# Performance work log

Measured on AMD Instinct MI355X. Metric: run time of the kernel, lower is better.

The kernel has to match this reference:

```python
import jax, jax.numpy as jnp
import numpy as np

B, C, H, W = 4, 192, 128, 128
HEADS = 4

def _conv1x1(x, w):
    # x: [B,Cin,H,W], w: [Cout,Cin,1,1]
    return jnp.einsum('bchw,oc->bohw', x, w[:, :, 0, 0])

def _dwconv3x3(x, w):
    # x: [B,C3,H,W], w: [C3,1,3,3], groups=C3
    return jax.lax.conv_general_dilated(
        x, w, window_strides=(1, 1), padding=((1, 1), (1, 1)),
        dimension_numbers=('NCHW', 'OIHW', 'NCHW'),
        feature_group_count=x.shape[1])

def setup_inputs() -> dict:
    key = jax.random.key(0)
    k1, k2, k3, k4 = jax.random.split(key, 4)
    return {
        'x': jax.random.normal(k1, (B, C, H, W), jnp.float32),
        'w_qkv': jax.random.normal(k2, (3 * C, C, 1, 1), jnp.float32) * 0.05,
        'w_dw': jax.random.normal(k3, (3 * C, 1, 3, 3), jnp.float32) * 0.1,
        'w_proj': jax.random.normal(k4, (C, C, 1, 1), jnp.float32) * 0.05,
        'temperature': jnp.ones((HEADS, 1, 1), jnp.float32),
    }

def reference(x, w_qkv, w_dw, w_proj, temperature):
    b, c, h, w = x.shape
    ch = c // HEADS  # channels per head
    qkv = _dwconv3x3(_conv1x1(x, w_qkv), w_dw)  # [B,3C,H,W]
    q, k, v = jnp.split(qkv, 3, axis=1)
    def heads(t):  # [B,C,H,W] -> [B,heads,ch,HW]
        return t.reshape(b, HEADS, ch, h * w)
    q, k, v = heads(q), heads(k), heads(v)
    # L2 normalize over spatial (token) axis
    q = q / jnp.maximum(jnp.linalg.norm(q, axis=-1, keepdims=True), 1e-12)
    k = k / jnp.maximum(jnp.linalg.norm(k, axis=-1, keepdims=True), 1e-12)
    attn = jnp.einsum('bhcn,bhdn->bhcd', q, k) * temperature[None]  # [B,heads,ch,ch]
    attn = jax.nn.softmax(attn, axis=-1)
    out = jnp.einsum('bhcd,bhdn->bhcn', attn, v)  # [B,heads,ch,HW]
    out = out.reshape(b, c, h, w)
    return _conv1x1(out, w_proj)
```

## Files before the change

kernel.cpp:

```cpp
#include <hip/hip_runtime.h>
#include <hip/hip_bf16.h>
#include <math.h>


#define B_ 4
#define C_ 192
#define H_ 128
#define W_ 128
#define HW_ 16384
#define HEADS_ 4
#define CH_ 48
#define CHUNKS_ 64

typedef __attribute__((ext_vector_type(8))) __bf16 bf16x8;
typedef __attribute__((ext_vector_type(8))) unsigned short u16x8;
typedef __attribute__((ext_vector_type(4))) float f32x4;

__device__ __forceinline__ unsigned short rne_bf16(float f) {
    unsigned int u = __float_as_uint(f);
    u += 0x7FFFu + ((u >> 16) & 1u);
    return (unsigned short)(u >> 16);
}
__device__ __forceinline__ float bf16_f32(unsigned short h) {
    return __uint_as_float(((unsigned int)h) << 16);
}

__global__ void k0_bf16(const float* __restrict__ wq,
                        unsigned short* __restrict__ wB, int n) {
    int idx = blockIdx.x * 256 + threadIdx.x;
    if (idx < n) wB[idx] = rne_bf16(wq[idx]);
}

__global__ __launch_bounds__(256, 3) void kg_f32(
    const unsigned short* __restrict__ A, int aStrideB,
    const float* __restrict__ X, unsigned short* __restrict__ Y) {
    __shared__ unsigned short AL[2][64 * 40];
    __shared__ unsigned short BL[2][256 * 40];
    int t = threadIdx.x;
    int wave = t >> 6, lane = t & 63;
    int lm = lane & 15, kg = lane >> 4;
    int p0 = blockIdx.x * 256;
    int m0 = blockIdx.y * 64;
    int b = blockIdx.z;
    const unsigned short* Ab = A + (size_t)b * aStrideB + (size_t)m0 * C_;
    const float* Xb = X + (size_t)b * C_ * HW_ + p0 + t;
    int ar = t >> 2, ac = (t & 3) * 8;
    size_t arow = (size_t)ar * C_ + ac;

    f32x4 acc[4][4];
#pragma unroll
    for (int mi = 0; mi < 4; ++mi)
#pragma unroll
        for (int ni = 0; ni < 4; ++ni) acc[mi][ni] = (f32x4)(0.f);

    float xv[32];
    u16x8 av;
#pragma unroll
    for (int i = 0; i < 32; ++i) xv[i] = Xb[(size_t)i * HW_];
    av = *(const u16x8*)&Ab[arow];
    *(u16x8*)&AL[0][ar * 40 + ac] = av;
#pragma unroll
    for (int c8 = 0; c8 < 4; ++c8) {
        u16x8 hh;
#pragma unroll
        for (int j = 0; j < 8; ++j) hh[j] = rne_bf16(xv[c8 * 8 + j]);
        *(u16x8*)&BL[0][t * 40 + c8 * 8] = hh;
    }
    __syncthreads();

    for (int s = 0; s < 6; ++s) {
        int cur = s & 1;
        if (s < 5) {
            int kn = (s + 1) * 32;
            const float* xp = Xb + (size_t)kn * HW_;
#pragma unroll
            for (int i = 0; i < 32; ++i) xv[i] = xp[(size_t)i * HW_];
            av = *(const u16x8*)&Ab[arow + kn];
        }
        bf16x8 fah[4], fbh[4];
#pragma unroll
        for (int mi = 0; mi < 4; ++mi) {
            int ro = (lm + mi * 16) * 40 + kg * 8;
            fah[mi] = __builtin_bit_cast(bf16x8, *(const u16x8*)&AL[cur][ro]);
        }
#pragma unroll
        for (int ni = 0; ni < 4; ++ni) {
            int ro = (wave * 64 + ni * 16 + lm) * 40 + kg * 8;
            fbh[ni] = __builtin_bit_cast(bf16x8, *(const u16x8*)&BL[cur][ro]);
        }
#pragma unroll
        for (int mi = 0; mi < 4; ++mi)
#pragma unroll
            for (int ni = 0; ni < 4; ++ni)
                acc[mi][ni] = __builtin_amdgcn_mfma_f32_16x16x32_bf16(
                    fah[mi], fbh[ni], acc[mi][ni], 0, 0, 0);
        if (s < 5) {
            int nxt = cur ^ 1;
            *(u16x8*)&AL[nxt][ar * 40 + ac] = av;
#pragma unroll
            for (int c8 = 0; c8 < 4; ++c8) {
                u16x8 hh;
#pragma unroll
                for (int j = 0; j < 8; ++j) hh[j] = rne_bf16(xv[c8 * 8 + j]);
                *(u16x8*)&BL[nxt][t * 40 + c8 * 8] = hh;
            }
        }
        __syncthreads();
    }
#pragma unroll
    for (int mi = 0; mi < 4; ++mi)
#pragma unroll
        for (int ni = 0; ni < 4; ++ni) {
            int oc = m0 + mi * 16 + kg * 4;
            int px = p0 + wave * 64 + ni * 16 + lm;
            unsigned short* yp = Y + ((size_t)b * C_ + oc) * HW_ + px;
#pragma unroll
            for (int r = 0; r < 4; ++r)
                yp[(size_t)r * HW_] = rne_bf16(acc[mi][ni][r]);
        }
}

__global__ __launch_bounds__(256, 3) void kg_b16(
    const unsigned short* __restrict__ A, int aStrideB,
    const unsigned short* __restrict__ X, float* __restrict__ Y) {
    __shared__ unsigned short AL[2][64 * 40];
    __shared__ unsigned short BL[2][256 * 40];
    int t = threadIdx.x;
    int wave = t >> 6, lane = t & 63;
    int lm = lane & 15, kg = lane >> 4;
    int p0 = blockIdx.x * 256;
    int m0 = blockIdx.y * 64;
    int b = blockIdx.z;
    const unsigned short* Ab = A + (size_t)b * aStrideB + (size_t)m0 * C_;
    const unsigned short* Xb = X + (size_t)b * C_ * HW_ + p0 + t;
    int ar = t >> 2, ac = (t & 3) * 8;
    size_t arow = (size_t)ar * C_ + ac;

    f32x4 acc[4][4];
#pragma unroll
    for (int mi = 0; mi < 4; ++mi)
#pragma unroll
        for (int ni = 0; ni < 4; ++ni) acc[mi][ni] = (f32x4)(0.f);

    unsigned short xv[32];
    u16x8 av;
#pragma unroll
    for (int i = 0; i < 32; ++i) xv[i] = Xb[(size_t)i * HW_];
    av = *(const u16x8*)&Ab[arow];
    *(u16x8*)&AL[0][ar * 40 + ac] = av;
#pragma unroll
    for (int c8 = 0; c8 < 4; ++c8) {
        u16x8 hh;
#pragma unroll
        for (int j = 0; j < 8; ++j) hh[j] = xv[c8 * 8 + j];
        *(u16x8*)&BL[0][t * 40 + c8 * 8] = hh;
    }
    __syncthreads();

    for (int s = 0; s < 6; ++s) {
        int cur = s & 1;
        if (s < 5) {
            int kn = (s + 1) * 32;
            const unsigned short* xp = Xb + (size_t)kn * HW_;
#pragma unroll
            for (int i = 0; i < 32; ++i) xv[i] = xp[(size_t)i * HW_];
            av = *(const u16x8*)&Ab[arow + kn];
        }
        bf16x8 fah[4], fbh[4];
#pragma unroll
        for (int mi = 0; mi < 4; ++mi) {
            int ro = (lm + mi * 16) * 40 + kg * 8;
            fah[mi] = __builtin_bit_cast(bf16x8, *(const u16x8*)&AL[cur][ro]);
        }
#pragma unroll
        for (int ni = 0; ni < 4; ++ni) {
            int ro = (wave * 64 + ni * 16 + lm) * 40 + kg * 8;
            fbh[ni] = __builtin_bit_cast(bf16x8, *(const u16x8*)&BL[cur][ro]);
        }
#pragma unroll
        for (int mi = 0; mi < 4; ++mi)
#pragma unroll
            for (int ni = 0; ni < 4; ++ni)
                acc[mi][ni] = __builtin_amdgcn_mfma_f32_16x16x32_bf16(
                    fah[mi], fbh[ni], acc[mi][ni], 0, 0, 0);
        if (s < 5) {
            int nxt = cur ^ 1;
            *(u16x8*)&AL[nxt][ar * 40 + ac] = av;
#pragma unroll
            for (int c8 = 0; c8 < 4; ++c8) {
                u16x8 hh;
#pragma unroll
                for (int j = 0; j < 8; ++j) hh[j] = xv[c8 * 8 + j];
                *(u16x8*)&BL[nxt][t * 40 + c8 * 8] = hh;
            }
        }
        __syncthreads();
    }
#pragma unroll
    for (int mi = 0; mi < 4; ++mi)
#pragma unroll
        for (int ni = 0; ni < 4; ++ni) {
            int oc = m0 + mi * 16 + kg * 4;
            int px = p0 + wave * 64 + ni * 16 + lm;
            float* yp = Y + ((size_t)b * C_ + oc) * HW_ + px;
#pragma unroll
            for (int r = 0; r < 4; ++r) yp[(size_t)r * HW_] = acc[mi][ni][r];
        }
}

__global__ __launch_bounds__(256, 6) void k2_dwconv(
    const unsigned short* __restrict__ y1, const float* __restrict__ wdw,
    unsigned short* __restrict__ dst, float* __restrict__ ssP, int g) {
    __shared__ float wss[4];
    int t = threadIdx.x;
    int c = blockIdx.y, b = blockIdx.z;
    int cg = (t & 31) * 4;
    int r0i = blockIdx.x * 32 + (t >> 5) * 4;
    const unsigned short* yp = y1 + ((size_t)b * C_ + c) * HW_;
    const float* wd = wdw + (size_t)(g * C_ + c) * 9;
    float w0 = wd[0], w1 = wd[1], w2 = wd[2];
    float w3 = wd[3], w4 = wd[4], w5 = wd[5];
    float w6 = wd[6], w7 = wd[7], w8 = wd[8];
    bool lv = cg > 0, rv = cg < W_ - 4;

    float4 mid[6];
    float lf[6], rt[6];
#pragma unroll
    for (int i = 0; i < 6; ++i) {
        int rr = r0i - 1 + i;
        if (rr >= 0 && rr < H_) {
            const unsigned short* rowp = yp + (size_t)rr * W_;
            ushort4 mv = *(const ushort4*)&rowp[cg];
            mid[i] = make_float4(bf16_f32(mv.x), bf16_f32(mv.y),
                                 bf16_f32(mv.z), bf16_f32(mv.w));
            lf[i] = lv ? bf16_f32(rowp[cg - 1]) : 0.f;
            rt[i] = rv ? bf16_f32(rowp[cg + 4]) : 0.f;
        } else {
            mid[i] = make_float4(0.f, 0.f, 0.f, 0.f);
            lf[i] = 0.f;
            rt[i] = 0.f;
        }
    }
    float ss = 0.f;
#pragma unroll
    for (int i = 0; i < 4; ++i) {
        float o0 = 0.f, o1 = 0.f, o2 = 0.f, o3 = 0.f;
#pragma unroll
        for (int k = 0; k < 3; ++k) {
            float4 m = mid[i + k];
            float L = lf[i + k], R = rt[i + k];
            float wa = (k == 0) ? w0 : (k == 1) ? w3 : w6;
            float wb = (k == 0) ? w1 : (k == 1) ? w4 : w7;
            float wc = (k == 0) ? w2 : (k == 1) ? w5 : w8;
            o0 = fmaf(wa, L,   fmaf(wb, m.x, fmaf(wc, m.y, o0)));
            o1 = fmaf(wa, m.x, fmaf(wb, m.y, fmaf(wc, m.z, o1)));
            o2 = fmaf(wa, m.y, fmaf(wb, m.z, fmaf(wc, m.w, o2)));
            o3 = fmaf(wa, m.z, fmaf(wb, m.w, fmaf(wc, R,   o3)));
        }
        unsigned short h0 = rne_bf16(o0), h1 = rne_bf16(o1);
        unsigned short h2 = rne_bf16(o2), h3 = rne_bf16(o3);
        float f0 = bf16_f32(h0), f1 = bf16_f32(h1);
        float f2 = bf16_f32(h2), f3 = bf16_f32(h3);
        ss += f0 * f0 + f1 * f1 + f2 * f2 + f3 * f3;
        size_t oi = ((size_t)b * C_ + c) * HW_ + (size_t)(r0i + i) * W_ + cg;
        ushort4 pk;
        pk.x = h0; pk.y = h1; pk.z = h2; pk.w = h3;
        *(ushort4*)&dst[oi] = pk;
    }
    if (ssP != nullptr) {
#pragma unroll
        for (int m = 32; m >= 1; m >>= 1) ss += __shfl_xor(ss, m, 64);
        if ((t & 63) == 0) wss[t >> 6] = ss;
        __syncthreads();
        if (t == 0)
            ssP[((size_t)b * C_ + c) * 4 + blockIdx.x] =
                (wss[0] + wss[1]) + (wss[2] + wss[3]);
    }
}

__global__ __launch_bounds__(256, 4) void k3_qk(
    const unsigned short* __restrict__ qp, const unsigned short* __restrict__ kp,
    float* __restrict__ Sp) {
    __shared__ unsigned int smem[9216];
    unsigned short* qh = (unsigned short*)smem;
    unsigned short* kh = qh + 6336;
    float* red = (float*)smem;
    int t = threadIdx.x;
    int w = t >> 6, lane = t & 63, lm = lane & 15, kg = lane >> 4;
    int chunk = blockIdx.x, h = blockIdx.y, b = blockIdx.z;
    const unsigned int* qb =
        (const unsigned int*)(qp + ((size_t)b * C_ + h * CH_) * HW_);
    const unsigned int* kb =
        (const unsigned int*)(kp + ((size_t)b * C_ + h * CH_) * HW_);

    f32x4 acc[3][3];
#pragma unroll
    for (int mi = 0; mi < 3; ++mi)
#pragma unroll
        for (int ni = 0; ni < 3; ++ni) acc[mi][ni] = (f32x4)(0.f);

    for (int s = 0; s < 2; ++s) {
        int base2 = (chunk * 256 + s * 128) >> 1;
        __syncthreads();
#pragma unroll
        for (int i = 0; i < 12; ++i) {
            int p = t + i * 256;
            int c = p >> 6, jp = p & 63;
            int da = c * 66 + jp;
            ((unsigned int*)qh)[da] = qb[(size_t)c * (HW_ / 2) + base2 + jp];
            ((unsigned int*)kh)[da] = kb[(size_t)c * (HW_ / 2) + base2 + jp];
        }
        __syncthreads();
        bf16x8 fqh[3], fkh[3];
#pragma unroll
        for (int mi = 0; mi < 3; ++mi) {
            int off = (lm + 16 * mi) * 132 + w * 32 + kg * 8;
            fqh[mi] = __builtin_bit_cast(bf16x8, *(const u16x8*)&qh[off]);
            fkh[mi] = __builtin_bit_cast(bf16x8, *(const u16x8*)&kh[off]);
        }
#pragma unroll
        for (int mi = 0; mi < 3; ++mi)
#pragma unroll
            for (int ni = 0; ni < 3; ++ni)
                acc[mi][ni] = __builtin_amdgcn_mfma_f32_16x16x32_bf16(
                    fqh[mi], fkh[ni], acc[mi][ni], 0, 0, 0);
    }
    __syncthreads();
#pragma unroll
    for (int mi = 0; mi < 3; ++mi)
#pragma unroll
        for (int ni = 0; ni < 3; ++ni) {
            int tile = mi * 3 + ni;
            *(f32x4*)&red[w * 2304 + tile * 256 + lane * 4] = acc[mi][ni];
        }
    __syncthreads();
    size_t ob = ((size_t)(b * HEADS_ + h) * CHUNKS_ + chunk) * 2304;
    for (int idx = t; idx < 2304; idx += 256) {
        float sv = (red[idx] + red[2304 + idx]) +
                   (red[4608 + idx] + red[6912 + idx]);
        int tile = idx >> 8, li = idx & 255;
        int ln = li >> 2, r = li & 3;
        int mi = tile / 3, ni = tile - mi * 3;
        int sidx = (mi * 16 + (ln >> 4) * 4 + r) * 48 + ni * 16 + (ln & 15);
        Sp[ob + sidx] = sv;
    }
}

__global__ __launch_bounds__(256, 4) void k4r_softmax(
    const float* __restrict__ Sp, const float* __restrict__ ssPq,
    const float* __restrict__ ssPk, const float* __restrict__ temp,
    float* __restrict__ P) {
    __shared__ float red[4][64];
    int t = threadIdx.x;
    int w = t >> 6, d = t & 63;
    int c = blockIdx.x, bh = blockIdx.y;
    int b = bh >> 2, h = bh & 3;
    float s = 0.f;
    if (d < 48) {
        const float* sp = Sp + (size_t)bh * CHUNKS_ * 2304 + c * 48 + d;
#pragma unroll
        for (int j = 0; j < 16; ++j)
            s += sp[(size_t)(w * 16 + j) * 2304];
    }
    red[w][d] = s;
    __syncthreads();
    if (w == 0) {
        float tot = (red[0][d] + red[1][d]) + (red[2][d] + red[3][d]);
        const float* spq = ssPq + ((size_t)b * C_ + h * CH_ + c) * 4;
        float rq = 1.f / fmaxf(
            sqrtf(fmaxf((spq[0] + spq[1]) + (spq[2] + spq[3]), 0.f)), 1e-12f);
        float logit = -1e30f;
        if (d < 48) {
            const float* spk = ssPk + ((size_t)b * C_ + h * CH_ + d) * 4;
            float rk = 1.f / fmaxf(
                sqrtf(fmaxf((spk[0] + spk[1]) + (spk[2] + spk[3]), 0.f)), 1e-12f);
            logit = tot * (rq * temp[h]) * rk;
        }
        float m = logit;
#pragma unroll
        for (int mm = 1; mm < 64; mm <<= 1) m = fmaxf(m, __shfl_xor(m, mm, 64));
        float e = (d < 48) ? expf(logit - m) : 0.f;
        float sum = e;
#pragma unroll
        for (int mm = 1; mm < 64; mm <<= 1) sum += __shfl_xor(sum, mm, 64);
        if (d < 48)
            P[(size_t)bh * 2304 + d * 48 + c] = e * (1.f / sum);
    }
}

__global__ __launch_bounds__(256, 2) void k4c_fold(
    const float* __restrict__ P, const float* __restrict__ wp,
    unsigned short* __restrict__ MTb) {
    __shared__ float sP[4 * 48 * 49];
    __shared__ float wpL[16 * 192];
    int t = threadIdx.x;
    int o0 = blockIdx.x * 16, b = blockIdx.y;
    const float* Pb = P + (size_t)b * 4 * 2304;
    for (int i = t; i < 4 * 2304; i += 256) {
        int h = i / 2304, rem = i - h * 2304;
        int d = rem / 48, cc = rem - d * 48;
        sP[h * 2352 + d * 49 + cc] = Pb[i];
    }
    for (int i = t; i < 16 * 192; i += 256) {
        int o = i / 192, cc = i - o * 192;
        wpL[i] = wp[(size_t)(o0 + o) * C_ + cc];
    }
    __syncthreads();
    for (int i = t; i < 16 * 192; i += 256) {
        int o = i / 192, cg = i - o * 192;
        int h = cg / 48, d = cg - h * 48;
        const float* wrow = &wpL[o * 192 + h * 48];
        const float* prow = &sP[h * 2352 + d * 49];
        float sum = 0.f;
#pragma unroll
        for (int c = 0; c < 48; ++c) sum = fmaf(wrow[c], prow[c], sum);
        MTb[((size_t)b * C_ + o0 + o) * C_ + cg] = rne_bf16(sum);
    }
}

extern "C" void kernel_launch(void* const* d_in, const int* in_sizes, int n_in,
                              void* d_out, int out_size, void* d_ws, size_t ws_size,
                              hipStream_t stream) {
    const float* x     = (const float*)d_in[0];
    const float* wqkv  = (const float*)d_in[1];
    const float* wdw   = (const float*)d_in[2];
    const float* wproj = (const float*)d_in[3];
    const float* temp  = (const float*)d_in[4];
    float* out = (float*)d_out;
    char* ws = (char*)d_ws;

    unsigned short* wqkvB = (unsigned short*)(ws + 0);
    unsigned short* MTb   = (unsigned short*)(ws + 221184);
    float* P    = (float*)(ws + 368640);
    float* ssPq = (float*)(ws + 516096);
    float* ssPk = (float*)(ws + 528384);
    unsigned short* y1 = (unsigned short*)(ws + 540672);
    float* Sp = (float*)(ws + 540672);
    unsigned short* q = (unsigned short*)(ws + 25706496);
    unsigned short* k = (unsigned short*)(ws + 50872320);
    unsigned short* v = q;

    hipLaunchKernelGGL(k0_bf16, dim3(432), dim3(256), 0, stream,
                       wqkv, wqkvB, 576 * 192);
    hipLaunchKernelGGL(kg_f32, dim3(64, 3, 4), dim3(256), 0, stream,
                       wqkvB, 0, x, y1);
    hipLaunchKernelGGL(k2_dwconv, dim3(4, 192, 4), dim3(256), 0, stream,
                       y1, wdw, q, ssPq, 0);
    hipLaunchKernelGGL(kg_f32, dim3(64, 3, 4), dim3(256), 0, stream,
                       wqkvB + 192 * 192, 0, x, y1);
    hipLaunchKernelGGL(k2_dwconv, dim3(4, 192, 4), dim3(256), 0, stream,
                       y1, wdw, k, ssPk, 1);
    hipLaunchKernelGGL(k3_qk, dim3(CHUNKS_, 4, 4), dim3(256), 0, stream, q, k, Sp);
    hipLaunchKernelGGL(k4r_softmax, dim3(48, 16), dim3(256), 0, stream,
                       Sp, ssPq, ssPk, temp, P);
    hipLaunchKernelGGL(k4c_fold, dim3(12, 4), dim3(256), 0, stream,
                       P, wproj, MTb);
    hipLaunchKernelGGL(kg_f32, dim3(64, 3, 4), dim3(256), 0, stream,
                       wqkvB + 2 * 192 * 192, 0, x, y1);
    hipLaunchKernelGGL(k2_dwconv, dim3(4, 192, 4), dim3(256), 0, stream,
                       y1, wdw, v, (float*)nullptr, 2);
    hipLaunchKernelGGL(kg_b16, dim3(64, 3, 4), dim3(256), 0, stream,
                       MTb, C_ * C_, v, out);
}
```

Baseline: 150.4 us.

## Batch Q/K/V projection and depthwise conv into single launches

The three per-projection 1x1-conv GEMM launches become one launch with a 9-block M dimension that writes a 576-channel intermediate. The three depthwise-conv launches become one kernel over all 576 channels, with sum-of-squares computed only for the q and k channels. This cuts four kernel launches and gives each launch a larger grid for better GPU fill. In exchange, the full q/k/v intermediate and output buffers are materialized at once, which raises the workspace footprint and the cache pressure compared with reusing one 192-channel scratch buffer.

```diff
diff --git a/kernel.cpp b/kernel.cpp
--- a/kernel.cpp
+++ b/kernel.cpp
@@ -5,6 +5,7 @@
 
 #define B_ 4
 #define C_ 192
+#define C3_ 576
 #define H_ 128
 #define W_ 128
 #define HW_ 16384
@@ -31,9 +32,9 @@
     if (idx < n) wB[idx] = rne_bf16(wq[idx]);
 }
 
-__global__ __launch_bounds__(256, 3) void kg_f32(
-    const unsigned short* __restrict__ A, int aStrideB,
-    const float* __restrict__ X, unsigned short* __restrict__ Y) {
+__global__ __launch_bounds__(256, 3) void kg_qkv(
+    const unsigned short* __restrict__ A, const float* __restrict__ X,
+    unsigned short* __restrict__ Y) {
     __shared__ unsigned short AL[2][64 * 40];
     __shared__ unsigned short BL[2][256 * 40];
     int t = threadIdx.x;
@@ -42,7 +43,7 @@
     int p0 = blockIdx.x * 256;
     int m0 = blockIdx.y * 64;
     int b = blockIdx.z;
-    const unsigned short* Ab = A + (size_t)b * aStrideB + (size_t)m0 * C_;
+    const unsigned short* Ab = A + (size_t)m0 * C_;
     const float* Xb = X + (size_t)b * C_ * HW_ + p0 + t;
     int ar = t >> 2, ac = (t & 3) * 8;
     size_t arow = (size_t)ar * C_ + ac;
@@ -113,7 +114,7 @@
         for (int ni = 0; ni < 4; ++ni) {
             int oc = m0 + mi * 16 + kg * 4;
             int px = p0 + wave * 64 + ni * 16 + lm;
-            unsigned short* yp = Y + ((size_t)b * C_ + oc) * HW_ + px;
+            unsigned short* yp = Y + ((size_t)b * C3_ + oc) * HW_ + px;
 #pragma unroll
             for (int r = 0; r < 4; ++r)
                 yp[(size_t)r * HW_] = rne_bf16(acc[mi][ni][r]);
@@ -121,8 +122,8 @@
 }
 
 __global__ __launch_bounds__(256, 3) void kg_b16(
-    const unsigned short* __restrict__ A, int aStrideB,
-    const unsigned short* __restrict__ X, float* __restrict__ Y) {
+    const unsigned short* __restrict__ A, const unsigned short* __restrict__ X,
+    float* __restrict__ Y) {
     __shared__ unsigned short AL[2][64 * 40];
     __shared__ unsigned short BL[2][256 * 40];
     int t = threadIdx.x;
@@ -131,8 +132,8 @@
     int p0 = blockIdx.x * 256;
     int m0 = blockIdx.y * 64;
     int b = blockIdx.z;
-    const unsigned short* Ab = A + (size_t)b * aStrideB + (size_t)m0 * C_;
-    const unsigned short* Xb = X + (size_t)b * C_ * HW_ + p0 + t;
+    const unsigned short* Ab = A + (size_t)b * C_ * C_ + (size_t)m0 * C_;
+    const unsigned short* Xb = X + (size_t)b * C3_ * HW_ + p0 + t;
     int ar = t >> 2, ac = (t & 3) * 8;
     size_t arow = (size_t)ar * C_ + ac;
 
@@ -208,16 +209,16 @@
         }
 }
 
-__global__ __launch_bounds__(256, 6) void k2_dwconv(
+__global__ __launch_bounds__(256, 6) void k2_all(
     const unsigned short* __restrict__ y1, const float* __restrict__ wdw,
-    unsigned short* __restrict__ dst, float* __restrict__ ssP, int g) {
+    unsigned short* __restrict__ qkv, float* __restrict__ ssQK) {
     __shared__ float wss[4];
     int t = threadIdx.x;
-    int c = blockIdx.y, b = blockIdx.z;
+    int gc = blockIdx.y, b = blockIdx.z;
     int cg = (t & 31) * 4;
     int r0i = blockIdx.x * 32 + (t >> 5) * 4;
-    const unsigned short* yp = y1 + ((size_t)b * C_ + c) * HW_;
-    const float* wd = wdw + (size_t)(g * C_ + c) * 9;
+    const unsigned short* yp = y1 + ((size_t)b * C3_ + gc) * HW_;
+    const float* wd = wdw + (size_t)gc * 9;
     float w0 = wd[0], w1 = wd[1], w2 = wd[2];
     float w3 = wd[3], w4 = wd[4], w5 = wd[5];
     float w6 = wd[6], w7 = wd[7], w8 = wd[8];
@@ -262,25 +263,24 @@
         float f0 = bf16_f32(h0), f1 = bf16_f32(h1);
         float f2 = bf16_f32(h2), f3 = bf16_f32(h3);
         ss += f0 * f0 + f1 * f1 + f2 * f2 + f3 * f3;
-        size_t oi = ((size_t)b * C_ + c) * HW_ + (size_t)(r0i + i) * W_ + cg;
+        size_t oi = ((size_t)b * C3_ + gc) * HW_ + (size_t)(r0i + i) * W_ + cg;
         ushort4 pk;
         pk.x = h0; pk.y = h1; pk.z = h2; pk.w = h3;
-        *(ushort4*)&dst[oi] = pk;
-    }
-    if (ssP != nullptr) {
+        *(ushort4*)&qkv[oi] = pk;
+    }
+    if (gc < 2 * C_) {
 #pragma unroll
         for (int m = 32; m >= 1; m >>= 1) ss += __shfl_xor(ss, m, 64);
         if ((t & 63) == 0) wss[t >> 6] = ss;
         __syncthreads();
         if (t == 0)
-            ssP[((size_t)b * C_ + c) * 4 + blockIdx.x] =
+            ssQK[((size_t)b * 2 * C_ + gc) * 4 + blockIdx.x] =
                 (wss[0] + wss[1]) + (wss[2] + wss[3]);
     }
 }
 
 __global__ __launch_bounds__(256, 4) void k3_qk(
-    const unsigned short* __restrict__ qp, const unsigned short* __restrict__ kp,
-    float* __restrict__ Sp) {
+    const unsigned short* __restrict__ qkv, float* __restrict__ Sp) {
     __shared__ unsigned int smem[9216];
     unsigned short* qh = (unsigned short*)smem;
     unsigned short* kh = qh + 6336;
@@ -289,9 +289,9 @@
     int w = t >> 6, lane = t & 63, lm = lane & 15, kg = lane >> 4;
     int chunk = blockIdx.x, h = blockIdx.y, b = blockIdx.z;
     const unsigned int* qb =
-        (const unsigned int*)(qp + ((size_t)b * C_ + h * CH_) * HW_);
+        (const unsigned int*)(qkv + ((size_t)b * C3_ + h * CH_) * HW_);
     const unsigned int* kb =
-        (const unsigned int*)(kp + ((size_t)b * C_ + h * CH_) * HW_);
+        (const unsigned int*)(qkv + ((size_t)b * C3_ + C_ + h * CH_) * HW_);
 
     f32x4 acc[3][3];
 #pragma unroll
@@ -347,9 +347,8 @@
 }
 
 __global__ __launch_bounds__(256, 4) void k4r_softmax(
-    const float* __restrict__ Sp, const float* __restrict__ ssPq,
-    const float* __restrict__ ssPk, const float* __restrict__ temp,
-    float* __restrict__ P) {
+    const float* __restrict__ Sp, const float* __restrict__ ssQK,
+    const float* __restrict__ temp, float* __restrict__ P) {
     __shared__ float red[4][64];
     int t = threadIdx.x;
     int w = t >> 6, d = t & 63;
@@ -366,12 +365,13 @@
     __syncthreads();
     if (w == 0) {
         float tot = (red[0][d] + red[1][d]) + (red[2][d] + red[3][d]);
-        const float* spq = ssPq + ((size_t)b * C_ + h * CH_ + c) * 4;
+        const float* spq = ssQK + ((size_t)b * 2 * C_ + h * CH_ + c) * 4;
         float rq = 1.f / fmaxf(
             sqrtf(fmaxf((spq[0] + spq[1]) + (spq[2] + spq[3]), 0.f)), 1e-12f);
         float logit = -1e30f;
         if (d < 48) {
-            const float* spk = ssPk + ((size_t)b * C_ + h * CH_ + d) * 4;
+            const float* spk =
+                ssQK + ((size_t)b * 2 * C_ + C_ + h * CH_ + d) * 4;
             float rk = 1.f / fmaxf(
                 sqrtf(fmaxf((spk[0] + spk[1]) + (spk[2] + spk[3]), 0.f)), 1e-12f);
             logit = tot * (rq * temp[h]) * rk;
@@ -432,33 +432,22 @@
     unsigned short* wqkvB = (unsigned short*)(ws + 0);
     unsigned short* MTb   = (unsigned short*)(ws + 221184);
     float* P    = (float*)(ws + 368640);
-    float* ssPq = (float*)(ws + 516096);
-    float* ssPk = (float*)(ws + 528384);
-    unsigned short* y1 = (unsigned short*)(ws + 540672);
+    float* ssQK = (float*)(ws + 516096);
+    unsigned short* y1qkv = (unsigned short*)(ws + 540672);
     float* Sp = (float*)(ws + 540672);
-    unsigned short* q = (unsigned short*)(ws + 25706496);
-    unsigned short* k = (unsigned short*)(ws + 50872320);
-    unsigned short* v = q;
+    unsigned short* qkv = (unsigned short*)(ws + 76038144);
 
     hipLaunchKernelGGL(k0_bf16, dim3(432), dim3(256), 0, stream,
                        wqkv, wqkvB, 576 * 192);
-    hipLaunchKernelGGL(kg_f32, dim3(64, 3, 4), dim3(256), 0, stream,
-                       wqkvB, 0, x, y1);
-    hipLaunchKernelGGL(k2_dwconv, dim3(4, 192, 4), dim3(256), 0, stream,
-                       y1, wdw, q, ssPq, 0);
-    hipLaunchKernelGGL(kg_f32, dim3(64, 3, 4), dim3(256), 0, stream,
-                       wqkvB + 192 * 192, 0, x, y1);
-    hipLaunchKernelGGL(k2_dwconv, dim3(4, 192, 4), dim3(256), 0, stream,
-                       y1, wdw, k, ssPk, 1);
-    hipLaunchKernelGGL(k3_qk, dim3(CHUNKS_, 4, 4), dim3(256), 0, stream, q, k, Sp);
+    hipLaunchKernelGGL(kg_qkv, dim3(64, 9, 4), dim3(256), 0, stream,
+                       wqkvB, x, y1qkv);
+    hipLaunchKernelGGL(k2_all, dim3(4, 576, 4), dim3(256), 0, stream,
+                       y1qkv, wdw, qkv, ssQK);
+    hipLaunchKernelGGL(k3_qk, dim3(CHUNKS_, 4, 4), dim3(256), 0, stream, qkv, Sp);
     hipLaunchKernelGGL(k4r_softmax, dim3(48, 16), dim3(256), 0, stream,
-                       Sp, ssPq, ssPk, temp, P);
+                       Sp, ssQK, temp, P);
     hipLaunchKernelGGL(k4c_fold, dim3(12, 4), dim3(256), 0, stream,
                        P, wproj, MTb);
-    hipLaunchKernelGGL(kg_f32, dim3(64, 3, 4), dim3(256), 0, stream,
-                       wqkvB + 2 * 192 * 192, 0, x, y1);
-    hipLaunchKernelGGL(k2_dwconv, dim3(4, 192, 4), dim3(256), 0, stream,
-                       y1, wdw, v, (float*)nullptr, 2);
     hipLaunchKernelGGL(kg_b16, dim3(64, 3, 4), dim3(256), 0, stream,
-                       MTb, C_ * C_, v, out);
-}
+                       MTb, qkv + (size_t)2 * C_ * HW_, out);
+}
```

Result: faster. 132.1 us, median of 2 (-12.2%).
